# Optimization experiments

Measured on AMD Instinct MI355X. Metric: run time of the kernel, lower is better.

## Reference

```python
import jax, jax.numpy as jnp
import numpy as np

T = 8192
INPUT = 1024
TRACE = 64
CTX = 16
OUT = 1024
EPS = 1e-5  # equinox LayerNorm default


def _linear(key, out_f, in_f):
    k1, k2 = jax.random.split(key)
    lim = 1.0 / np.sqrt(in_f)
    w = jax.random.uniform(k1, (out_f, in_f), minval=-lim, maxval=lim, dtype=jnp.float32)
    b = jax.random.uniform(k2, (out_f,), minval=-lim, maxval=lim, dtype=jnp.float32)
    return w, b


def setup_inputs() -> dict:
    key = jax.random.key(0)
    ks = jax.random.split(key, 8)
    x = jax.random.normal(ks[0], (T, INPUT), dtype=jnp.float32)
    start = jax.random.randint(ks[1], (T,), 0, 2).astype(bool)
    next_done = jax.random.randint(ks[2], (T,), 0, 2).astype(bool)
    state_re = jnp.zeros((1, TRACE, CTX), dtype=jnp.float32)
    state_im = jnp.zeros((1, TRACE, CTX), dtype=jnp.float32)
    pre_w, pre_b = _linear(ks[3], TRACE, INPUT)
    gi_w, gi_b = _linear(ks[4], TRACE, INPUT)
    go_w, go_b = _linear(ks[5], OUT, INPUT)
    skip_w, skip_b = _linear(ks[6], OUT, INPUT)
    mix_w, mix_b = _linear(ks[7], OUT, 2 * TRACE * CTX)
    # ffa.init: deterministic decay rates a and oscillation freqs b
    ffa_a = jnp.linspace(1e-6, 0.5, TRACE, dtype=jnp.float32)
    ffa_b = (2.0 * jnp.pi / jnp.exp(jnp.linspace(jnp.log(1.0), jnp.log(1024.0), CTX))).astype(jnp.float32)
    return dict(x=x, state_re=state_re, state_im=state_im, start=start, next_done=next_done,
                pre_w=pre_w, pre_b=pre_b, gi_w=gi_w, gi_b=gi_b, go_w=go_w, go_b=go_b,
                skip_w=skip_w, skip_b=skip_b, mix_w=mix_w, mix_b=mix_b,
                ffa_a=ffa_a, ffa_b=ffa_b)


def _ffa_apply(ffa_a, ffa_b, gated_x, state0, start):
    """Resettable complex linear recurrence: s_t = gamma * s_{t-1} + x_t, reset at episode starts.
    gamma = exp(-|a| + i b), outer over (trace, context). Parallelized with an associative scan
    over monoid elements (reset_flag, state, elapsed_steps)."""
    Tn, m = gated_x.shape
    c = ffa_b.shape[0]
    ab = jax.lax.complex(
        jnp.broadcast_to(-jnp.abs(ffa_a)[None, :, None], (1, m, c)),
        jnp.broadcast_to(ffa_b[None, None, :], (1, m, c)),
    )  # [1, m, c] complex: log-gamma per unit timestep

    xc = jnp.broadcast_to(gated_x[:, :, None].astype(jnp.complex64), (Tn, m, c))
    # prepend carried-in recurrent state: timestep 0, no reset
    x_e = jnp.concatenate([state0.astype(jnp.complex64), xc], axis=0)          # [T+1, m, c]
    s_e = jnp.concatenate([jnp.zeros((1, 1, 1), bool), start[:, None, None]], axis=0)
    i_e = jnp.concatenate([jnp.zeros((1, 1, 1), jnp.float32),
                           jnp.ones((Tn, 1, 1), jnp.float32)], axis=0)

    def op(a, b):
        s1, x1, i1 = a
        s2, x2, i2 = b
        # zero the carried state across episode boundaries
        x1 = jnp.where(s2, 0.0, x1)
        i1 = jnp.where(s2, 0.0, i1)
        g = jnp.exp(ab * i2.astype(jnp.complex64))  # decay over i2 elapsed steps
        return (jnp.logical_or(s1, s2), x1 * g + x2, i1 + i2)

    _, states, _ = jax.lax.associative_scan(op, (s_e, x_e, i_e), axis=0)
    return states[1:]  # [T, m, c] complex64


def reference(x, state_re, state_im, start, next_done,
              pre_w, pre_b, gi_w, gi_b, go_w, go_b,
              skip_w, skip_b, mix_w, mix_b, ffa_a, ffa_b):
    gate_in = jax.nn.sigmoid(x @ gi_w.T + gi_b)          # [T, trace]
    pre = x @ pre_w.T + pre_b                            # [T, trace]
    gated_x = pre * gate_in

    state0 = jax.lax.complex(state_re, state_im)         # [1, trace, ctx]
    state = _ffa_apply(ffa_a, ffa_b, gated_x, state0, start)  # [T, trace, ctx] complex

    z_in = jnp.concatenate([jnp.real(state), jnp.imag(state)], axis=-1)
    z_in = z_in.reshape(state.shape[0], -1)              # [T, 2*trace*ctx]
    z = z_in @ mix_w.T + mix_b                           # [T, out]

    gate_out = jax.nn.sigmoid(x @ go_w.T + go_b)         # [T, out]
    skip = x @ skip_w.T + skip_b                         # [T, out]

    zg = z * gate_out
    mu = zg.mean(-1, keepdims=True)
    var = ((zg - mu) ** 2).mean(-1, keepdims=True)
    ln = (zg - mu) / jnp.sqrt(var + EPS)                 # LayerNorm, no affine

    out = ln + skip * (1.0 - gate_out)
    final_state = state[-1:]
    return out, final_state


if __name__ == "__main__":
    inp = setup_inputs()
    out, fs = jax.jit(reference)(**inp)
    print(out.shape, out.dtype, fs.shape, fs.dtype)
```

## Files before the change

kernel.cpp:

```cpp
#include <hip/hip_runtime.h>
#include <math.h>

#define T_DIM 8192
#define IN_DIM 1024
#define TRACE 64
#define CTX 16
#define OUT_DIM 1024
#define KMIX 2048

typedef __attribute__((ext_vector_type(8))) short bf16x8;
typedef __attribute__((ext_vector_type(4))) float f32x4;
typedef __attribute__((ext_vector_type(16))) float f32x16;

__device__ __forceinline__ unsigned short f2bf(float f) {
    unsigned int u = __float_as_uint(f);
    u = (u + 0x7FFFu + ((u >> 16) & 1u)) >> 16;
    return (unsigned short)u;
}
__device__ __forceinline__ float bf2f(unsigned short b) {
    return __uint_as_float(((unsigned int)b) << 16);
}

__device__ __forceinline__ void gl2lds16(const void* g, void* l) {
    __builtin_amdgcn_global_load_lds(
        (const __attribute__((address_space(1))) unsigned int*)g,
        (__attribute__((address_space(3))) unsigned int*)l,
        16, 0, 0);
}


__global__ __launch_bounds__(256) void c0_conv(const float* __restrict__ x,
        const float* __restrict__ gw, const float* __restrict__ sw, const float* __restrict__ mw,
        const float* __restrict__ pw, const float* __restrict__ giw,
        const void* __restrict__ startp,
        unsigned short* __restrict__ xb, unsigned short* __restrict__ gob,
        unsigned short* __restrict__ skb, unsigned short* __restrict__ mixb,
        unsigned short* __restrict__ pwb, unsigned short* __restrict__ gwb,
        unsigned char* __restrict__ mask, unsigned long long* __restrict__ mask64)
{
    if (blockIdx.x == 0) {
        __shared__ int nonbool;
        int tid = threadIdx.x;
        if (tid == 0) nonbool = 0;
        __syncthreads();
        const unsigned int* wv = (const unsigned int*)startp;
        #pragma unroll
        for (int p = 0; p < 8; p++) {
            unsigned int a = wv[tid * 8 + p];
            if (a > 1u) nonbool = 1;
        }
        __syncthreads();
        if (nonbool) {
            const unsigned char* s8 = (const unsigned char*)startp;
            for (int i = tid; i < T_DIM; i += 256) mask[i] = (unsigned char)(s8[i] != 0);
        } else {
            const int* s32 = (const int*)startp;
            for (int i = tid; i < T_DIM; i += 256) mask[i] = (unsigned char)(s32[i] != 0);
        }
        __syncthreads();
        if (tid < 128) {
            unsigned long long wv2 = 0ull;
            int base = tid * 64;
            #pragma unroll 8
            for (int b2 = 0; b2 < 64; b2++)
                wv2 |= ((unsigned long long)(mask[base + b2] & 1)) << b2;
            mask64[tid] = wv2;
        }
    }
    const size_t QX = 2097152, QG = 262144, QS = 262144, QP = 16384, QI = 16384;
    const size_t totalA = QX + QG + QS + QP + QI;
    for (size_t q = (size_t)blockIdx.x * blockDim.x + threadIdx.x; q < totalA;
         q += (size_t)gridDim.x * blockDim.x) {
        const float* src; unsigned short* dst; size_t i;
        if (q < QX)               { src = x;   dst = xb;   i = q; }
        else if (q < QX+QG)       { src = gw;  dst = gob;  i = q - QX; }
        else if (q < QX+QG+QS)    { src = sw;  dst = skb;  i = q - QX - QG; }
        else if (q < QX+QG+QS+QP) { src = pw;  dst = pwb;  i = q - QX - QG - QS; }
        else                      { src = giw; dst = gwb;  i = q - QX - QG - QS - QP; }
        float4 v = *(const float4*)(src + i * 4);
        ushort4 o;
        o.x = f2bf(v.x); o.y = f2bf(v.y); o.z = f2bf(v.z); o.w = f2bf(v.w);
        *(ushort4*)(dst + i * 4) = o;
    }
    const size_t QM = 524288;
    for (size_t q = (size_t)blockIdx.x * blockDim.x + threadIdx.x; q < QM;
         q += (size_t)gridDim.x * blockDim.x) {
        float4 v = *(const float4*)(mw + q * 4);
        int flat = (int)(q * 4);
        int n  = flat >> 11;
        int kk = flat & 2047;
        int mm = kk >> 5;
        int w_ = kk & 31;
        int p  = w_ >> 4;
        int cc = w_ & 15;
        int kb = (n << 11) + mm * 32 + (cc << 1) + p;
        mixb[kb]     = f2bf(v.x);
        mixb[kb + 2] = f2bf(v.y);
        mixb[kb + 4] = f2bf(v.z);
        mixb[kb + 6] = f2bf(v.w);
    }
}

__global__ __launch_bounds__(256) void k1_mfma(const unsigned short* __restrict__ xb,
        const unsigned short* __restrict__ pwb, const unsigned short* __restrict__ gwb,
        const float* __restrict__ pre_b, const float* __restrict__ gi_b,
        float* __restrict__ gxT)
{
    __shared__ __align__(16) unsigned short As[1024];
    __shared__ __align__(16) unsigned short Bs[4096];
    __shared__ float sgE[64][33];

    const int tid = threadIdx.x;
    const int t0 = blockIdx.x * 32;
    const int lane = tid & 63, w = tid >> 6;
    const int quad = lane >> 4, l16 = lane & 15;
    const int r = tid >> 2, s4 = tid & 3;
    const int csw = (s4 - ((r >> 1) & 3)) & 3;

    f32x4 acc[2][2];
    const f32x4 zero4 = {0.f, 0.f, 0.f, 0.f};
    #pragma unroll
    for (int mi = 0; mi < 2; mi++)
        #pragma unroll
        for (int ni = 0; ni < 2; ni++) acc[mi][ni] = zero4;

    const int sfr = (quad + ((l16 >> 1) & 3)) & 3;

    for (int k0 = 0; k0 < IN_DIM; k0 += 32) {
        __syncthreads();
        if (tid < 128) {
            int ra = tid >> 2;
            int ca = ((tid & 3) - ((ra >> 1) & 3)) & 3;
            gl2lds16(xb + (size_t)(t0 + ra) * IN_DIM + k0 + ca * 8, As + tid * 8);
        }
        gl2lds16(pwb + (size_t)r * IN_DIM + k0 + csw * 8, Bs + tid * 8);
        gl2lds16(gwb + (size_t)r * IN_DIM + k0 + csw * 8, Bs + 2048 + tid * 8);
        asm volatile("s_waitcnt vmcnt(0)" ::: "memory");
        __syncthreads();
        bf16x8 af[2], bf[2];
        #pragma unroll
        for (int mi = 0; mi < 2; mi++)
            af[mi] = *(const bf16x8*)&As[(mi * 16 + l16) * 32 + sfr * 8];
        #pragma unroll
        for (int ni = 0; ni < 2; ni++)
            bf[ni] = *(const bf16x8*)&Bs[(w * 32 + ni * 16 + l16) * 32 + sfr * 8];
        #pragma unroll
        for (int mi = 0; mi < 2; mi++)
            #pragma unroll
            for (int ni = 0; ni < 2; ni++)
                acc[mi][ni] = __builtin_amdgcn_mfma_f32_16x16x32_bf16(af[mi], bf[ni], acc[mi][ni], 0, 0, 0);
    }

    if (w >= 2) {
        #pragma unroll
        for (int mi = 0; mi < 2; mi++)
            #pragma unroll
            for (int ni = 0; ni < 2; ni++) {
                int mg = (w - 2) * 32 + ni * 16 + l16;
                float gb = gi_b[mg];
                #pragma unroll
                for (int rr = 0; rr < 4; rr++) {
                    int tl = mi * 16 + quad * 4 + rr;
                    sgE[mg][tl] = 1.f / (1.f + expf(-(acc[mi][ni][rr] + gb)));
                }
            }
    }
    __syncthreads();
    if (w < 2) {
        #pragma unroll
        for (int mi = 0; mi < 2; mi++)
            #pragma unroll
            for (int ni = 0; ni < 2; ni++) {
                int mp = w * 32 + ni * 16 + l16;
                float pb = pre_b[mp];
                float4 o;
                float* po = &o.x;
                #pragma unroll
                for (int rr = 0; rr < 4; rr++) {
                    int tl = mi * 16 + quad * 4 + rr;
                    po[rr] = (acc[mi][ni][rr] + pb) * sgE[mp][tl];
                }
                *(float4*)&gxT[(size_t)mp * T_DIM + t0 + mi * 16 + quad * 4] = o;
            }
    }
}

__global__ __launch_bounds__(1024, 1) void k2_scan(const float* __restrict__ gxT,
        const unsigned long long* __restrict__ mask64,
        const float* __restrict__ state_re, const float* __restrict__ state_im,
        const float* __restrict__ ffa_a, const float* __restrict__ ffa_b,
        unsigned short* __restrict__ zinb, float* __restrict__ fstate)
{
    const int m  = blockIdx.x >> 2;
    const int qd = blockIdx.x & 3;
    const int tid = threadIdx.x;
    const int c = tid & 15, j = tid >> 4;
    __shared__ __align__(16) float gxs[8192 + 128];
    __shared__ float Br[16][65], Bi[16][65], Er[16][65], Ei[16][65];
    __shared__ unsigned char Rf[16][65];
    __shared__ float B32r[16][16][3], B32i[16][16][3];
    __shared__ unsigned char sRf[16][16][3];

    const float am = -fabsf(ffa_a[m]);
    const float bc = ffa_b[c];
    const float er = expf(am);
    const float gr = er * cosf(bc);
    const float gi = er * sinf(bc);

    {
        const float4* gx4 = (const float4*)(gxT + (size_t)m * T_DIM);
        #pragma unroll
        for (int it = 0; it < 2; it++) {
            int g = it * 1024 + tid;
            float4 v = gx4[g];
            int t = g * 4;
            gxs[t     + ( t      >> 6)] = v.x;
            gxs[t + 1 + ((t + 1) >> 6)] = v.y;
            gxs[t + 2 + ((t + 2) >> 6)] = v.z;
            gxs[t + 3 + ((t + 3) >> 6)] = v.w;
        }
    }
    const unsigned long long mw0 = mask64[j * 2];
    const unsigned long long mw1 = mask64[j * 2 + 1];
    __syncthreads();

    const int lb = j * 130;
    const int gloc = j - qd * 16;
    const bool own = (unsigned)gloc < 16u;

    float sre = 0.f, sim = 0.f;
    #pragma unroll 8
    for (int i = 0; i < 32; i++) {
        if ((mw0 >> i) & 1ull) { sre = 0.f; sim = 0.f; }
        else { float tr_ = sre * gr - sim * gi; sim = sre * gi + sim * gr; sre = tr_; }
        sre += gxs[lb + i];
    }
    if (own) { B32r[c][gloc][0] = sre; B32i[c][gloc][0] = sim;
               sRf[c][gloc][0] = ((mw0 & 0xffffffffull) != 0ull) ? 1 : 0; }
    #pragma unroll 8
    for (int i = 0; i < 32; i++) {
        if ((mw0 >> (i + 32)) & 1ull) { sre = 0.f; sim = 0.f; }
        else { float tr_ = sre * gr - sim * gi; sim = sre * gi + sim * gr; sre = tr_; }
        sre += gxs[lb + 32 + i];
    }
    if (own) { B32r[c][gloc][1] = sre; B32i[c][gloc][1] = sim;
               sRf[c][gloc][1] = (mw0 != 0ull) ? 1 : 0; }
    #pragma unroll 8
    for (int i = 0; i < 32; i++) {
        if ((mw1 >> i) & 1ull) { sre = 0.f; sim = 0.f; }
        else { float tr_ = sre * gr - sim * gi; sim = sre * gi + sim * gr; sre = tr_; }
        sre += gxs[lb + 65 + i];
    }
    if (own) { B32r[c][gloc][2] = sre; B32i[c][gloc][2] = sim;
               sRf[c][gloc][2] = ((mw0 != 0ull) || ((mw1 & 0xffffffffull) != 0ull)) ? 1 : 0; }
    #pragma unroll 8
    for (int i = 0; i < 32; i++) {
        if ((mw1 >> (i + 32)) & 1ull) { sre = 0.f; sim = 0.f; }
        else { float tr_ = sre * gr - sim * gi; sim = sre * gi + sim * gr; sre = tr_; }
        sre += gxs[lb + 97 + i];
    }
    Br[c][j] = sre; Bi[c][j] = sim; Rf[c][j] = ((mw0 | mw1) != 0ull) ? 1 : 0;
    __syncthreads();

    if (tid < 16) {
        const int cc = tid;
        float b2 = 128.f * ffa_b[cc];
        float e128 = expf(128.f * am);
        float gRr = e128 * cosf(b2);
        float gRi = e128 * sinf(b2);
        float pr = state_re[m * CTX + cc], pi = state_im[m * CTX + cc];
        for (int q2 = 0; q2 < 64; q2++) {
            Er[cc][q2] = pr; Ei[cc][q2] = pi;
            if (Rf[cc][q2]) { pr = Br[cc][q2]; pi = Bi[cc][q2]; }
            else {
                float nr = pr * gRr - pi * gRi + Br[cc][q2];
                pi       = pr * gRi + pi * gRr + Bi[cc][q2];
                pr = nr;
            }
        }
    }
    __syncthreads();

    {
        const int gl2 = j >> 2, s = j & 3;
        const int g = qd * 16 + gl2;
        const unsigned long long w0 = mask64[g * 2];
        const unsigned long long w1 = mask64[g * 2 + 1];
        const unsigned int mbits = (unsigned int)(((s < 2) ? w0 : w1) >> ((s & 1) * 32));
        float str, sti;
        {
            float E_r = Er[c][g], E_i = Ei[c][g];
            if (s == 0) { str = E_r; sti = E_i; }
            else if (sRf[c][gl2][s - 1]) { str = B32r[c][gl2][s - 1]; sti = B32i[c][gl2][s - 1]; }
            else {
                float ang = 32.f * (float)s * bc;
                float mag = expf(32.f * (float)s * am);
                float gsr = mag * cosf(ang), gsi = mag * sinf(ang);
                str = B32r[c][gl2][s - 1] + E_r * gsr - E_i * gsi;
                sti = B32i[c][gl2][s - 1] + E_r * gsi + E_i * gsr;
            }
        }
        const int pb = g * 130 + (s >> 1) * 65 + (s & 1) * 32;
        const int tstart = g * 128 + s * 32;
        unsigned int* zout = (unsigned int*)zinb;
        const int obase = m * CTX + c;
        #pragma unroll 8
        for (int i = 0; i < 32; i++) {
            if ((mbits >> i) & 1u) { str = 0.f; sti = 0.f; }
            else { float tr_ = str * gr - sti * gi; sti = str * gi + sti * gr; str = tr_; }
            str += gxs[pb + i];
            unsigned int u = (unsigned int)f2bf(str) | ((unsigned int)f2bf(sti) << 16);
            zout[((size_t)(tstart + i) << 10) + obase] = u;
        }
        if (qd == 3 && j == 63) {
            fstate[obase]        = str;
            fstate[1024 + obase] = sti;
        }
    }
}

__global__ __launch_bounds__(512, 2) void gA_gemm(
        const unsigned short* __restrict__ xb,   const unsigned short* __restrict__ zinb,
        const unsigned short* __restrict__ gob,  const unsigned short* __restrict__ skb,
        const unsigned short* __restrict__ mixb,
        const float* __restrict__ go_b, const float* __restrict__ skip_b, const float* __restrict__ mix_b,
        unsigned short* __restrict__ zg, unsigned short* __restrict__ sk2)
{
    __shared__ __align__(16) unsigned short L[49152];
    const int tid = threadIdx.x;
    const int b = blockIdx.x;
    const int xcd = b & 7, q = b >> 3;
    const int t0 = (xcd * 4 + (q >> 3)) * 256;
    const int n0 = (q & 7) * 128;

    const int lane = tid & 63, w = tid >> 6;
    const int wm = w >> 1, wn = w & 1;
    const int l31 = lane & 31, h = lane >> 5;
    const int r = tid >> 2;
    const int csw = ((tid & 3) - ((r >> 1) & 3)) & 3;
    const int c8 = csw * 8;
    const int srot = (l31 >> 1) & 3;
    const int dst8 = tid * 8;

    f32x16 accg[2][2], acck[2][2];
    #pragma unroll
    for (int mi = 0; mi < 2; mi++)
        #pragma unroll
        for (int ni = 0; ni < 2; ni++)
            #pragma unroll
            for (int e = 0; e < 16; e++) { accg[mi][ni][e] = 0.f; acck[mi][ni][e] = 0.f; }

    {
        const unsigned short* gA0 = xb  + (size_t)(t0 + r)       * IN_DIM + c8;
        const unsigned short* gA1 = xb  + (size_t)(t0 + 128 + r) * IN_DIM + c8;
        const unsigned short* gB0 = gob + (size_t)(n0 + r)       * IN_DIM + c8;
        const unsigned short* gC0 = skb + (size_t)(n0 + r)       * IN_DIM + c8;

#define STAGE_F(bufi, kof) do {                         \
        unsigned short* _b = &L[(bufi) * 16384];        \
        gl2lds16(gA0 + (kof), _b + dst8);               \
        gl2lds16(gA1 + (kof), _b + 4096 + dst8);        \
        gl2lds16(gB0 + (kof), _b + 8192 + dst8);        \
        gl2lds16(gC0 + (kof), _b + 12288 + dst8);       \
    } while (0)

#define STEP_F(T, CUR, NXT, DOST, VMC) do {             \
        const unsigned short* As = &L[(CUR) * 16384];   \
        const unsigned short* Bs = As + 8192;           \
        const unsigned short* Cs = As + 12288;          \
        _Pragma("unroll")                               \
        for (int kh = 0; kh < 2; kh++) {                \
            const int so = ((kh * 2 + h + srot) & 3) * 8; \
            bf16x8 af[2], bg[2], bk[2];                 \
            _Pragma("unroll")                           \
            for (int mi = 0; mi < 2; mi++)              \
                af[mi] = *(const bf16x8*)&As[(wm * 64 + mi * 32 + l31) * 32 + so]; \
            _Pragma("unroll")                           \
            for (int ni = 0; ni < 2; ni++) {            \
                bg[ni] = *(const bf16x8*)&Bs[(wn * 64 + ni * 32 + l31) * 32 + so]; \
                bk[ni] = *(const bf16x8*)&Cs[(wn * 64 + ni * 32 + l31) * 32 + so]; \
            }                                           \
            if (kh == 0 && (DOST)) STAGE_F(NXT, ((T) + 2) * 32); \
            __builtin_amdgcn_s_setprio(1);              \
            _Pragma("unroll")                           \
            for (int mi = 0; mi < 2; mi++)              \
                _Pragma("unroll")                       \
                for (int ni = 0; ni < 2; ni++) {        \
                    accg[mi][ni] = __builtin_amdgcn_mfma_f32_32x32x16_bf16(af[mi], bg[ni], accg[mi][ni], 0, 0, 0); \
                    acck[mi][ni] = __builtin_amdgcn_mfma_f32_32x32x16_bf16(af[mi], bk[ni], acck[mi][ni], 0, 0, 0); \
                }                                       \
            __builtin_amdgcn_s_setprio(0);              \
        }                                               \
        asm volatile("s_waitcnt vmcnt(" #VMC ")" ::: "memory"); \
        __builtin_amdgcn_s_barrier();                   \
    } while (0)

        STAGE_F(0, 0);
        STAGE_F(1, 32);
        asm volatile("s_waitcnt vmcnt(4)" ::: "memory");
        __builtin_amdgcn_s_barrier();

        for (int t3i = 0; t3i < 30; t3i += 3) {
            STEP_F(t3i,     0, 2, 1, 4);
            STEP_F(t3i + 1, 1, 0, 1, 4);
            STEP_F(t3i + 2, 2, 1, 1, 4);
        }
        STEP_F(30, 0, 2, 0, 0);
        STEP_F(31, 1, 0, 0, 0);
#undef STEP_F
#undef STAGE_F
    }

    unsigned int sigp[32];
    #pragma unroll
    for (int mi = 0; mi < 2; mi++)
        #pragma unroll
        for (int ni = 0; ni < 2; ni++) {
            int n = n0 + wn * 64 + ni * 32 + l31;
            float gb = go_b[n];
            float sb_ = skip_b[n];
            #pragma unroll
            for (int reg = 0; reg < 16; reg++) {
                int row = (reg & 3) + 8 * (reg >> 2) + 4 * h;
                int t = t0 + wm * 64 + mi * 32 + row;
                float s = 1.f / (1.f + expf(-(accg[mi][ni][reg] + gb)));
                sk2[(size_t)t * OUT_DIM + n] = f2bf((acck[mi][ni][reg] + sb_) * (1.f - s));
                unsigned int pk = (unsigned int)f2bf(s);
                int idx = (mi * 2 + ni) * 8 + (reg >> 1);
                if (reg & 1) sigp[idx] |= pk << 16;
                else         sigp[idx]  = pk;
            }
        }

    #pragma unroll
    for (int mi = 0; mi < 2; mi++)
        #pragma unroll
        for (int ni = 0; ni < 2; ni++)
            #pragma unroll
            for (int e = 0; e < 16; e++) accg[mi][ni][e] = 0.f;
    {
        const unsigned short* mA0 = zinb + (size_t)(t0 + r)       * KMIX + c8;
        const unsigned short* mA1 = zinb + (size_t)(t0 + 128 + r) * KMIX + c8;
        const unsigned short* mB0 = mixb + (size_t)(n0 + r)       * KMIX + c8;

#define STAGE_M(bufi, kof) do {                         \
        unsigned short* _b = &L[(bufi) * 16384];        \
        gl2lds16(mA0 + (kof), _b + dst8);               \
        gl2lds16(mA1 + (kof), _b + 4096 + dst8);        \
        gl2lds16(mB0 + (kof), _b + 8192 + dst8);        \
    } while (0)

#define STEP_M(T, CUR, NXT, DOST, VMC) do {             \
        const unsigned short* As = &L[(CUR) * 16384];   \
        const unsigned short* Bs = As + 8192;           \
        _Pragma("unroll")                               \
        for (int kh = 0; kh < 2; kh++) {                \
            const int so = ((kh * 2 + h + srot) & 3) * 8; \
            bf16x8 af[2], bf[2];                        \
            _Pragma("unroll")                           \
            for (int mi = 0; mi < 2; mi++)              \
                af[mi] = *(const bf16x8*)&As[(wm * 64 + mi * 32 + l31) * 32 + so]; \
            _Pragma("unroll")                           \
            for (int ni = 0; ni < 2; ni++)              \
                bf[ni] = *(const bf16x8*)&Bs[(wn * 64 + ni * 32 + l31) * 32 + so]; \
            if (kh == 0 && (DOST)) STAGE_M(NXT, ((T) + 2) * 32); \
            __builtin_amdgcn_s_setprio(1);              \
            _Pragma("unroll")                           \
            for (int mi = 0; mi < 2; mi++)              \
                _Pragma("unroll")                       \
                for (int ni = 0; ni < 2; ni++)          \
                    accg[mi][ni] = __builtin_amdgcn_mfma_f32_32x32x16_bf16(af[mi], bf[ni], accg[mi][ni], 0, 0, 0); \
            __builtin_amdgcn_s_setprio(0);              \
        }                                               \
        asm volatile("s_waitcnt vmcnt(" #VMC ")" ::: "memory"); \
        __builtin_amdgcn_s_barrier();                   \
    } while (0)

        STAGE_M(0, 0);
        STAGE_M(1, 32);
        asm volatile("s_waitcnt vmcnt(3)" ::: "memory");
        __builtin_amdgcn_s_barrier();

        for (int t3i = 0; t3i < 60; t3i += 3) {
            STEP_M(t3i,     0, 2, 1, 3);
            STEP_M(t3i + 1, 1, 0, 1, 3);
            STEP_M(t3i + 2, 2, 1, 1, 3);
        }
        STEP_M(60, 0, 2, 1, 3);
        STEP_M(61, 1, 0, 1, 3);
        STEP_M(62, 2, 1, 0, 0);
        STEP_M(63, 0, 2, 0, 0);
#undef STEP_M
#undef STAGE_M
    }

    #pragma unroll
    for (int mi = 0; mi < 2; mi++)
        #pragma unroll
        for (int ni = 0; ni < 2; ni++) {
            int n = n0 + wn * 64 + ni * 32 + l31;
            float mb_ = mix_b[n];
            #pragma unroll
            for (int reg = 0; reg < 16; reg++) {
                int row = (reg & 3) + 8 * (reg >> 2) + 4 * h;
                int t = t0 + wm * 64 + mi * 32 + row;
                unsigned int u = sigp[(mi * 2 + ni) * 8 + (reg >> 1)];
                float sig = bf2f((unsigned short)((reg & 1) ? (u >> 16) : (u & 0xffff)));
                zg[(size_t)t * OUT_DIM + n] = f2bf((accg[mi][ni][reg] + mb_) * sig);
            }
        }
}

__global__ __launch_bounds__(256) void g3_ln(const unsigned short* __restrict__ zg,
        const unsigned short* __restrict__ sk2, const float* __restrict__ fstate,
        float* __restrict__ out, int out_size)
{
    __shared__ float sb[4], qb[4];
    __shared__ float mu_s, rstd_s;
    const int t = blockIdx.x;
    const int tid = threadIdx.x;
    ushort4 zu = *(const ushort4*)&zg [(size_t)t * OUT_DIM + tid * 4];
    ushort4 su = *(const ushort4*)&sk2[(size_t)t * OUT_DIM + tid * 4];
    float z0 = bf2f(zu.x), z1 = bf2f(zu.y), z2 = bf2f(zu.z), z3 = bf2f(zu.w);
    float s0 = bf2f(su.x), s1 = bf2f(su.y), s2 = bf2f(su.z), s3 = bf2f(su.w);
    float s = z0 + z1 + z2 + z3;
    float q = z0*z0 + z1*z1 + z2*z2 + z3*z3;
    #pragma unroll
    for (int off = 32; off > 0; off >>= 1) {
        s += __shfl_down(s, off, 64);
        q += __shfl_down(q, off, 64);
    }
    int wid = tid >> 6;
    if ((tid & 63) == 0) { sb[wid] = s; qb[wid] = q; }
    __syncthreads();
    if (tid == 0) {
        float S = sb[0] + sb[1] + sb[2] + sb[3];
        float Q = qb[0] + qb[1] + qb[2] + qb[3];
        float mu = S * (1.f / 1024.f);
        float var = Q * (1.f / 1024.f) - mu * mu;
        mu_s = mu; rstd_s = rsqrtf(var + 1e-5f);
    }
    __syncthreads();
    float mu = mu_s, rs = rstd_s;
    float4 o;
    o.x = (z0 - mu) * rs + s0;
    o.y = (z1 - mu) * rs + s1;
    o.z = (z2 - mu) * rs + s2;
    o.w = (z3 - mu) * rs + s3;
    *(float4*)&out[(size_t)t * OUT_DIM + tid * 4] = o;

    if (t < 8) {
        int i = t * 256 + tid;
        long long base = (long long)T_DIM * OUT_DIM;
        if (base + i < (long long)out_size) out[base + i] = fstate[i];
    }
}

extern "C" void kernel_launch(void* const* d_in, const int* in_sizes, int n_in,
                              void* d_out, int out_size, void* d_ws, size_t ws_size,
                              hipStream_t stream) {
    const float* x        = (const float*)d_in[0];
    const float* state_re = (const float*)d_in[1];
    const float* state_im = (const float*)d_in[2];
    const void*  startp   = d_in[3];
    const float* pre_w    = (const float*)d_in[5];
    const float* pre_b    = (const float*)d_in[6];
    const float* gi_w     = (const float*)d_in[7];
    const float* gi_b     = (const float*)d_in[8];
    const float* go_w     = (const float*)d_in[9];
    const float* go_b     = (const float*)d_in[10];
    const float* skip_w   = (const float*)d_in[11];
    const float* skip_b   = (const float*)d_in[12];
    const float* mix_w    = (const float*)d_in[13];
    const float* mix_b    = (const float*)d_in[14];
    const float* ffa_a    = (const float*)d_in[15];
    const float* ffa_b    = (const float*)d_in[16];

    float* ws = (float*)d_ws;
    float*          gxT    = ws;
    unsigned short* zinb   = (unsigned short*)(ws + 8912896);
    unsigned short* xb     = (unsigned short*)(ws + 17301504);
    unsigned short* gob    = (unsigned short*)(ws + 21495808);
    unsigned short* skb    = (unsigned short*)(ws + 22020096);
    unsigned short* mixb   = (unsigned short*)(ws + 22544384);
    unsigned short* zg     = (unsigned short*)(ws + 23592960);
    unsigned short* sk2    = (unsigned short*)(ws + 27787264);
    float*          fstate = ws + 31981568;
    unsigned char*  mask   = (unsigned char*)(ws + 31983616);
    unsigned long long* mask64 = (unsigned long long*)(ws + 31985664);
    unsigned short* pwb    = zg;
    unsigned short* gwb    = zg + 65536;
    float* out = (float*)d_out;

    hipLaunchKernelGGL(c0_conv,  dim3(1536), dim3(256),  0, stream, x, go_w, skip_w, mix_w, pre_w, gi_w,
                                                          startp, xb, gob, skb, mixb, pwb, gwb, mask, mask64);
    hipLaunchKernelGGL(k1_mfma,  dim3(256),  dim3(256),  0, stream, xb, pwb, gwb, pre_b, gi_b, gxT);
    hipLaunchKernelGGL(k2_scan,  dim3(256),  dim3(1024), 0, stream, gxT, mask64, state_re, state_im, ffa_a, ffa_b, zinb, fstate);
    hipLaunchKernelGGL(gA_gemm,  dim3(256),  dim3(512),  0, stream, xb, zinb, gob, skb, mixb, go_b, skip_b, mix_b, zg, sk2);
    hipLaunchKernelGGL(g3_ln,    dim3(8192), dim3(256),  0, stream, zg, sk2, fstate, out, out_size);
}
```

Before: 257.0 us.

## Pre-swizzle weight operands into MFMA fragment order and load B directly to registers

The go/skip/mix weight conversions now write bf16 data in a tiled layout that matches the per-lane MFMA B-fragment order. The fused GEMM kernel then loads B fragments straight from global memory into registers, prefetched one k-step ahead, and stages only the activation tile through LDS. This roughly halves LDS usage and removes the LDS reads for B, which may allow higher occupancy. In exchange it costs more VGPRs for the register prefetch, and B global loads are no longer shared across waves.

```diff
diff --git a/kernel.cpp b/kernel.cpp
--- a/kernel.cpp
+++ b/kernel.cpp
@@ -67,20 +67,34 @@
             mask64[tid] = wv2;
         }
     }
-    const size_t QX = 2097152, QG = 262144, QS = 262144, QP = 16384, QI = 16384;
-    const size_t totalA = QX + QG + QS + QP + QI;
+    const size_t QX = 2097152, QP = 16384, QI = 16384;
+    const size_t totalA = QX + QP + QI;
     for (size_t q = (size_t)blockIdx.x * blockDim.x + threadIdx.x; q < totalA;
          q += (size_t)gridDim.x * blockDim.x) {
         const float* src; unsigned short* dst; size_t i;
-        if (q < QX)               { src = x;   dst = xb;   i = q; }
-        else if (q < QX+QG)       { src = gw;  dst = gob;  i = q - QX; }
-        else if (q < QX+QG+QS)    { src = sw;  dst = skb;  i = q - QX - QG; }
-        else if (q < QX+QG+QS+QP) { src = pw;  dst = pwb;  i = q - QX - QG - QS; }
-        else                      { src = giw; dst = gwb;  i = q - QX - QG - QS - QP; }
+        if (q < QX)          { src = x;   dst = xb;  i = q; }
+        else if (q < QX+QP)  { src = pw;  dst = pwb; i = q - QX; }
+        else                 { src = giw; dst = gwb; i = q - QX - QP; }
         float4 v = *(const float4*)(src + i * 4);
         ushort4 o;
         o.x = f2bf(v.x); o.y = f2bf(v.y); o.z = f2bf(v.z); o.w = f2bf(v.w);
         *(ushort4*)(dst + i * 4) = o;
+    }
+    const size_t QG = 262144;
+    for (size_t q = (size_t)blockIdx.x * blockDim.x + threadIdx.x; q < 2 * QG;
+         q += (size_t)gridDim.x * blockDim.x) {
+        const float* src = (q < QG) ? gw : sw;
+        unsigned short* dst = (q < QG) ? gob : skb;
+        size_t i = (q < QG) ? q : q - QG;
+        float4 v = *(const float4*)(src + i * 4);
+        int flat = (int)(i * 4);
+        int n = flat >> 10;
+        int k = flat & 1023;
+        int D = (n >> 5) * 32768 + (k >> 5) * 1024 + ((k >> 4) & 1) * 512
+              + ((k >> 3) & 1) * 256 + (n & 31) * 8 + (k & 7);
+        ushort4 o;
+        o.x = f2bf(v.x); o.y = f2bf(v.y); o.z = f2bf(v.z); o.w = f2bf(v.w);
+        *(ushort4*)(dst + D) = o;
     }
     const size_t QM = 524288;
     for (size_t q = (size_t)blockIdx.x * blockDim.x + threadIdx.x; q < QM;
@@ -93,11 +107,13 @@
         int w_ = kk & 31;
         int p  = w_ >> 4;
         int cc = w_ & 15;
-        int kb = (n << 11) + mm * 32 + (cc << 1) + p;
-        mixb[kb]     = f2bf(v.x);
-        mixb[kb + 2] = f2bf(v.y);
-        mixb[kb + 4] = f2bf(v.z);
-        mixb[kb + 6] = f2bf(v.w);
+        int w2 = 2 * cc + p;
+        int D = (n >> 5) * 65536 + mm * 1024 + (w2 >> 4) * 512
+              + ((w2 >> 3) & 1) * 256 + (n & 31) * 8 + (w2 & 7);
+        mixb[D]     = f2bf(v.x);
+        mixb[D + 2] = f2bf(v.y);
+        mixb[D + 4] = f2bf(v.z);
+        mixb[D + 6] = f2bf(v.w);
     }
 }
 
@@ -326,7 +342,7 @@
         const float* __restrict__ go_b, const float* __restrict__ skip_b, const float* __restrict__ mix_b,
         unsigned short* __restrict__ zg, unsigned short* __restrict__ sk2)
 {
-    __shared__ __align__(16) unsigned short L[49152];
+    __shared__ __align__(16) unsigned short L[24576];
     const int tid = threadIdx.x;
     const int b = blockIdx.x;
     const int xcd = b & 7, q = b >> 3;
@@ -350,66 +366,76 @@
             #pragma unroll
             for (int e = 0; e < 16; e++) { accg[mi][ni][e] = 0.f; acck[mi][ni][e] = 0.f; }
 
-    {
-        const unsigned short* gA0 = xb  + (size_t)(t0 + r)       * IN_DIM + c8;
-        const unsigned short* gA1 = xb  + (size_t)(t0 + 128 + r) * IN_DIM + c8;
-        const unsigned short* gB0 = gob + (size_t)(n0 + r)       * IN_DIM + c8;
-        const unsigned short* gC0 = skb + (size_t)(n0 + r)       * IN_DIM + c8;
-
-#define STAGE_F(bufi, kof) do {                         \
-        unsigned short* _b = &L[(bufi) * 16384];        \
-        gl2lds16(gA0 + (kof), _b + dst8);               \
-        gl2lds16(gA1 + (kof), _b + 4096 + dst8);        \
-        gl2lds16(gB0 + (kof), _b + 8192 + dst8);        \
-        gl2lds16(gC0 + (kof), _b + 12288 + dst8);       \
+    bf16x8 bgR[2][2], bkR[2][2];
+
+    const unsigned short* bgB[2];
+    const unsigned short* bkB[2];
+    #pragma unroll
+    for (int ni = 0; ni < 2; ni++) {
+        int grp = (n0 >> 5) + wn * 2 + ni;
+        bgB[ni] = gob + (size_t)grp * 32768 + lane * 8;
+        bkB[ni] = skb + (size_t)grp * 32768 + lane * 8;
+    }
+
+    const unsigned short* gA0 = xb + (size_t)(t0 + r)       * IN_DIM + c8;
+    const unsigned short* gA1 = xb + (size_t)(t0 + 128 + r) * IN_DIM + c8;
+
+#define STAGE_A(bufi, kof, P0, P1) do {                       \
+        unsigned short* _b = &L[(bufi) * 8192];               \
+        gl2lds16(P0 + (kof), _b + dst8);                      \
+        gl2lds16(P1 + (kof), _b + 4096 + dst8);               \
     } while (0)
 
-#define STEP_F(T, CUR, NXT, DOST, VMC) do {             \
-        const unsigned short* As = &L[(CUR) * 16384];   \
-        const unsigned short* Bs = As + 8192;           \
-        const unsigned short* Cs = As + 12288;          \
-        _Pragma("unroll")                               \
-        for (int kh = 0; kh < 2; kh++) {                \
-            const int so = ((kh * 2 + h + srot) & 3) * 8; \
-            bf16x8 af[2], bg[2], bk[2];                 \
-            _Pragma("unroll")                           \
-            for (int mi = 0; mi < 2; mi++)              \
-                af[mi] = *(const bf16x8*)&As[(wm * 64 + mi * 32 + l31) * 32 + so]; \
-            _Pragma("unroll")                           \
-            for (int ni = 0; ni < 2; ni++) {            \
-                bg[ni] = *(const bf16x8*)&Bs[(wn * 64 + ni * 32 + l31) * 32 + so]; \
-                bk[ni] = *(const bf16x8*)&Cs[(wn * 64 + ni * 32 + l31) * 32 + so]; \
-            }                                           \
-            if (kh == 0 && (DOST)) STAGE_F(NXT, ((T) + 2) * 32); \
-            __builtin_amdgcn_s_setprio(1);              \
-            _Pragma("unroll")                           \
-            for (int mi = 0; mi < 2; mi++)              \
-                _Pragma("unroll")                       \
-                for (int ni = 0; ni < 2; ni++) {        \
-                    accg[mi][ni] = __builtin_amdgcn_mfma_f32_32x32x16_bf16(af[mi], bg[ni], accg[mi][ni], 0, 0, 0); \
-                    acck[mi][ni] = __builtin_amdgcn_mfma_f32_32x32x16_bf16(af[mi], bk[ni], acck[mi][ni], 0, 0, 0); \
-                }                                       \
-            __builtin_amdgcn_s_setprio(0);              \
-        }                                               \
+#define BLOAD_F(T) do {                                       \
+        _Pragma("unroll")                                     \
+        for (int ni = 0; ni < 2; ni++)                        \
+            _Pragma("unroll")                                 \
+            for (int kh = 0; kh < 2; kh++) {                  \
+                bgR[ni][kh] = *(const bf16x8*)(bgB[ni] + (T) * 1024 + kh * 512); \
+                bkR[ni][kh] = *(const bf16x8*)(bkB[ni] + (T) * 1024 + kh * 512); \
+            }                                                 \
+    } while (0)
+
+#define STEP_F(T, CUR, NXT, DOST, DOB, VMC) do {              \
+        const unsigned short* As = &L[(CUR) * 8192];          \
+        bf16x8 af[2][2];                                      \
+        _Pragma("unroll")                                     \
+        for (int mi = 0; mi < 2; mi++)                        \
+            _Pragma("unroll")                                 \
+            for (int kh = 0; kh < 2; kh++)                    \
+                af[mi][kh] = *(const bf16x8*)&As[(wm * 64 + mi * 32 + l31) * 32 + ((kh * 2 + h + srot) & 3) * 8]; \
+        if (DOST) STAGE_A(NXT, ((T) + 2) * 32, gA0, gA1);     \
+        __builtin_amdgcn_s_setprio(1);                        \
+        _Pragma("unroll")                                     \
+        for (int mi = 0; mi < 2; mi++)                        \
+            _Pragma("unroll")                                 \
+            for (int ni = 0; ni < 2; ni++) {                  \
+                accg[mi][ni] = __builtin_amdgcn_mfma_f32_32x32x16_bf16(af[mi][0], bgR[ni][0], accg[mi][ni], 0, 0, 0); \
+                acck[mi][ni] = __builtin_amdgcn_mfma_f32_32x32x16_bf16(af[mi][0], bkR[ni][0], acck[mi][ni], 0, 0, 0); \
+                accg[mi][ni] = __builtin_amdgcn_mfma_f32_32x32x16_bf16(af[mi][1], bgR[ni][1], accg[mi][ni], 0, 0, 0); \
+                acck[mi][ni] = __builtin_amdgcn_mfma_f32_32x32x16_bf16(af[mi][1], bkR[ni][1], acck[mi][ni], 0, 0, 0); \
+            }                                                 \
+        __builtin_amdgcn_s_setprio(0);                        \
+        if (DOB) BLOAD_F((T) + 1);                            \
         asm volatile("s_waitcnt vmcnt(" #VMC ")" ::: "memory"); \
-        __builtin_amdgcn_s_barrier();                   \
+        __builtin_amdgcn_s_barrier();                         \
     } while (0)
 
-        STAGE_F(0, 0);
-        STAGE_F(1, 32);
-        asm volatile("s_waitcnt vmcnt(4)" ::: "memory");
-        __builtin_amdgcn_s_barrier();
-
-        for (int t3i = 0; t3i < 30; t3i += 3) {
-            STEP_F(t3i,     0, 2, 1, 4);
-            STEP_F(t3i + 1, 1, 0, 1, 4);
-            STEP_F(t3i + 2, 2, 1, 1, 4);
-        }
-        STEP_F(30, 0, 2, 0, 0);
-        STEP_F(31, 1, 0, 0, 0);
+    STAGE_A(0, 0, gA0, gA1);
+    STAGE_A(1, 32, gA0, gA1);
+    BLOAD_F(0);
+    asm volatile("s_waitcnt vmcnt(10)" ::: "memory");
+    __builtin_amdgcn_s_barrier();
+
+    for (int t3i = 0; t3i < 30; t3i += 3) {
+        STEP_F(t3i,     0, 2, 1, 1, 10);
+        STEP_F(t3i + 1, 1, 0, 1, 1, 10);
+        STEP_F(t3i + 2, 2, 1, 1, 1, 10);
+    }
+    STEP_F(30, 0, 2, 0, 1, 8);
+    STEP_F(31, 1, 0, 0, 0, 0);
 #undef STEP_F
-#undef STAGE_F
-    }
+#undef BLOAD_F
 
     unsigned int sigp[32];
     #pragma unroll
@@ -438,61 +464,65 @@
         for (int ni = 0; ni < 2; ni++)
             #pragma unroll
             for (int e = 0; e < 16; e++) accg[mi][ni][e] = 0.f;
-    {
-        const unsigned short* mA0 = zinb + (size_t)(t0 + r)       * KMIX + c8;
-        const unsigned short* mA1 = zinb + (size_t)(t0 + 128 + r) * KMIX + c8;
-        const unsigned short* mB0 = mixb + (size_t)(n0 + r)       * KMIX + c8;
-
-#define STAGE_M(bufi, kof) do {                         \
-        unsigned short* _b = &L[(bufi) * 16384];        \
-        gl2lds16(mA0 + (kof), _b + dst8);               \
-        gl2lds16(mA1 + (kof), _b + 4096 + dst8);        \
-        gl2lds16(mB0 + (kof), _b + 8192 + dst8);        \
+
+    const unsigned short* mA0 = zinb + (size_t)(t0 + r)       * KMIX + c8;
+    const unsigned short* mA1 = zinb + (size_t)(t0 + 128 + r) * KMIX + c8;
+    const unsigned short* bfB[2];
+    #pragma unroll
+    for (int ni = 0; ni < 2; ni++) {
+        int grp = (n0 >> 5) + wn * 2 + ni;
+        bfB[ni] = mixb + (size_t)grp * 65536 + lane * 8;
+    }
+
+#define BLOAD_M(T) do {                                       \
+        _Pragma("unroll")                                     \
+        for (int ni = 0; ni < 2; ni++)                        \
+            _Pragma("unroll")                                 \
+            for (int kh = 0; kh < 2; kh++)                    \
+                bgR[ni][kh] = *(const bf16x8*)(bfB[ni] + (T) * 1024 + kh * 512); \
     } while (0)
 
-#define STEP_M(T, CUR, NXT, DOST, VMC) do {             \
-        const unsigned short* As = &L[(CUR) * 16384];   \
-        const unsigned short* Bs = As + 8192;           \
-        _Pragma("unroll")                               \
-        for (int kh = 0; kh < 2; kh++) {                \
-            const int so = ((kh * 2 + h + srot) & 3) * 8; \
-            bf16x8 af[2], bf[2];                        \
-            _Pragma("unroll")                           \
-            for (int mi = 0; mi < 2; mi++)              \
-                af[mi] = *(const bf16x8*)&As[(wm * 64 + mi * 32 + l31) * 32 + so]; \
-            _Pragma("unroll")                           \
-            for (int ni = 0; ni < 2; ni++)              \
-                bf[ni] = *(const bf16x8*)&Bs[(wn * 64 + ni * 32 + l31) * 32 + so]; \
-            if (kh == 0 && (DOST)) STAGE_M(NXT, ((T) + 2) * 32); \
-            __builtin_amdgcn_s_setprio(1);              \
-            _Pragma("unroll")                           \
-            for (int mi = 0; mi < 2; mi++)              \
-                _Pragma("unroll")                       \
-                for (int ni = 0; ni < 2; ni++)          \
-                    accg[mi][ni] = __builtin_amdgcn_mfma_f32_32x32x16_bf16(af[mi], bf[ni], accg[mi][ni], 0, 0, 0); \
-            __builtin_amdgcn_s_setprio(0);              \
-        }                                               \
+#define STEP_M(T, CUR, NXT, DOST, DOB, VMC) do {              \
+        const unsigned short* As = &L[(CUR) * 8192];          \
+        bf16x8 af[2][2];                                      \
+        _Pragma("unroll")                                     \
+        for (int mi = 0; mi < 2; mi++)                        \
+            _Pragma("unroll")                                 \
+            for (int kh = 0; kh < 2; kh++)                    \
+                af[mi][kh] = *(const bf16x8*)&As[(wm * 64 + mi * 32 + l31) * 32 + ((kh * 2 + h + srot) & 3) * 8]; \
+        if (DOST) STAGE_A(NXT, ((T) + 2) * 32, mA0, mA1);     \
+        __builtin_amdgcn_s_setprio(1);                        \
+        _Pragma("unroll")                                     \
+        for (int mi = 0; mi < 2; mi++)                        \
+            _Pragma("unroll")                                 \
+            for (int ni = 0; ni < 2; ni++) {                  \
+                accg[mi][ni] = __builtin_amdgcn_mfma_f32_32x32x16_bf16(af[mi][0], bgR[ni][0], accg[mi][ni], 0, 0, 0); \
+                accg[mi][ni] = __builtin_amdgcn_mfma_f32_32x32x16_bf16(af[mi][1], bgR[ni][1], accg[mi][ni], 0, 0, 0); \
+            }                                                 \
+        __builtin_amdgcn_s_setprio(0);                        \
+        if (DOB) BLOAD_M((T) + 1);                            \
         asm volatile("s_waitcnt vmcnt(" #VMC ")" ::: "memory"); \
-        __builtin_amdgcn_s_barrier();                   \
+        __builtin_amdgcn_s_barrier();                         \
     } while (0)
 
-        STAGE_M(0, 0);
-        STAGE_M(1, 32);
-        asm volatile("s_waitcnt vmcnt(3)" ::: "memory");
-        __builtin_amdgcn_s_barrier();
-
-        for (int t3i = 0; t3i < 60; t3i += 3) {
-            STEP_M(t3i,     0, 2, 1, 3);
-            STEP_M(t3i + 1, 1, 0, 1, 3);
-            STEP_M(t3i + 2, 2, 1, 1, 3);
-        }
-        STEP_M(60, 0, 2, 1, 3);
-        STEP_M(61, 1, 0, 1, 3);
-        STEP_M(62, 2, 1, 0, 0);
-        STEP_M(63, 0, 2, 0, 0);
+    STAGE_A(0, 0, mA0, mA1);
+    STAGE_A(1, 32, mA0, mA1);
+    BLOAD_M(0);
+    asm volatile("s_waitcnt vmcnt(6)" ::: "memory");
+    __builtin_amdgcn_s_barrier();
+
+    for (int t3i = 0; t3i < 60; t3i += 3) {
+        STEP_M(t3i,     0, 2, 1, 1, 6);
+        STEP_M(t3i + 1, 1, 0, 1, 1, 6);
+        STEP_M(t3i + 2, 2, 1, 1, 1, 6);
+    }
+    STEP_M(60, 0, 2, 1, 1, 6);
+    STEP_M(61, 1, 0, 1, 1, 6);
+    STEP_M(62, 2, 1, 0, 1, 4);
+    STEP_M(63, 0, 2, 0, 0, 0);
 #undef STEP_M
-#undef STAGE_M
-    }
+#undef BLOAD_M
+#undef STAGE_A
 
     #pragma unroll
     for (int mi = 0; mi < 2; mi++)
```

New measurement: 288.2 us. 12.1% more time.
